# Optimization experiments

Hardware: AMD Instinct MI355X
Metric: run time of the kernel (lower is better)

The kernel has to match this reference:

```python
import jax, jax.numpy as jnp
import numpy as np

EPS = 1e-7  # K.epsilon()
ROUTINGS = 3


def squash(v, axis=-1):
    s2 = jnp.sum(jnp.square(v), axis=axis, keepdims=True)
    scale = s2 / (1.0 + s2) / jnp.sqrt(s2 + EPS)
    return scale * v


def setup_inputs() -> dict:
    key = jax.random.key(0)
    k1, k2 = jax.random.split(key)
    B, I, D, O, K = 64, 2048, 8, 32, 16
    x = jax.random.normal(k1, (B, I, D), dtype=jnp.float32)
    W = jax.random.normal(k2, (I, O, D, K), dtype=jnp.float32) * 0.05
    return {"x": x, "W": W}


def reference(x, W):
    # u_hat[b,o,i,k] = sum_d x[b,i,d] * W[i,o,d,k]
    u_hat = jnp.einsum('bid,iodk->boik', x, W)  # [B, O, I, K]
    B, O, I, _ = u_hat.shape
    b = jnp.zeros((B, O, I), dtype=u_hat.dtype)
    v = None
    for i in range(ROUTINGS):
        c = jax.nn.softmax(b, axis=1)                      # over output capsules
        s = jnp.einsum('boi,boik->bok', c, u_hat)          # weighted sum
        v = squash(s)                                      # [B, O, K]
        if i < ROUTINGS - 1:
            agreement = jnp.einsum('boik,bok->boi', u_hat, v)
            b = b + agreement
    return v
```

## Files before the change

kernel.cpp:

```cpp
#include <hip/hip_runtime.h>
#include <hip/hip_fp16.h>


typedef _Float16 hf2 __attribute__((ext_vector_type(2)));

struct __align__(16) H8 { __half2 a, b, c, d; };
struct __align__(8)  H4 { __half2 a, b; };

__device__ __forceinline__ float dot2(hf2 a, hf2 b, float c) {
#if __has_builtin(__builtin_amdgcn_fdot2)
    return __builtin_amdgcn_fdot2(a, b, c, false);
#else
    return fmaf((float)a.x, (float)b.x, fmaf((float)a.y, (float)b.y, c));
#endif
}

template<int CTRL>
__device__ __forceinline__ float dppadd(float v) {
    return v + __int_as_float(__builtin_amdgcn_update_dpp(
        0, __float_as_int(v), CTRL, 0xF, 0xF, true));
}

__global__ __launch_bounds__(512)
void prep_kernel(const float* __restrict__ W, float* __restrict__ W16)
{
    const int ch = blockIdx.x;
    const int t  = threadIdx.x;
    const int is = t >> 6, l = t & 63, o = l & 31, kk = l >> 5;
    const int i  = ch * 8 + is;

    const float* wp = W + (size_t)(i * 32 + o) * 128 + kk * 8;
    float r[8][8];
    #pragma unroll
    for (int d = 0; d < 8; ++d) {
        float4 a = *(const float4*)(wp + d * 16);
        float4 b = *(const float4*)(wp + d * 16 + 4);
        r[d][0] = a.x; r[d][1] = a.y; r[d][2] = a.z; r[d][3] = a.w;
        r[d][4] = b.x; r[d][5] = b.y; r[d][6] = b.z; r[d][7] = b.w;
    }
    float4* dst = (float4*)W16 + (size_t)i * 512 + l;
    #pragma unroll
    for (int j = 0; j < 8; ++j) {
        float o4[4];
        #pragma unroll
        for (int d2 = 0; d2 < 4; ++d2) {
            hf2 p; p.x = (_Float16)r[2 * d2][j]; p.y = (_Float16)r[2 * d2 + 1][j];
            o4[d2] = __builtin_bit_cast(float, p);
        }
        dst[(size_t)j * 64] = make_float4(o4[0], o4[1], o4[2], o4[3]);
    }
}

template<int PASS0>
__global__ __launch_bounds__(512, 6)
void pass_kernel(const float* __restrict__ x,
                 const float* __restrict__ W16,
                 const __half* __restrict__ vin,
                 __half* __restrict__ part)
{
    __shared__ __align__(16) hf2    x_ldsh[16][8][4];
    __shared__ __align__(16) __half redh[2][16][512];

    const int t  = threadIdx.x;
    const int w  = t >> 6;
    const int l  = t & 63;
    const int o  = l & 31;
    const int kk = l >> 5;
    const int bx = blockIdx.x;
    const int ch = bx & 255;
    const int qh = bx >> 8;

    float Whf[4][8];
    {
        const float4* wp = (const float4*)W16 + (size_t)(ch * 8 + w) * 512 + l;
        #pragma unroll
        for (int j = 0; j < 8; ++j) {
            float4 ld = wp[(size_t)j * 64];
            Whf[0][j] = ld.x; Whf[1][j] = ld.y; Whf[2][j] = ld.z; Whf[3][j] = ld.w;
        }
        #pragma unroll
        for (int d2 = 0; d2 < 4; ++d2)
            #pragma unroll
            for (int j = 0; j < 8; ++j)
                asm volatile("" : "+v"(Whf[d2][j]));
    }
    {
        const int bl = t >> 5, wv = (t >> 2) & 7, d2 = t & 3;
        const float2 xx = *(const float2*)(
            x + (size_t)(qh * 16 + bl) * 16384 + (size_t)(ch * 8 + wv) * 8 + 2 * d2);
        hf2 p; p.x = (_Float16)xx.x; p.y = (_Float16)xx.y;
        x_ldsh[bl][wv][d2] = p;
    }

    #pragma unroll 2
    for (int g = 0; g < 8; ++g) {
        __syncthreads();

        if (g && t < 256) {
            const int bqf = t >> 7;
            const int hx  = (t & 127) * 4;
            const __half* rp = &redh[(g - 1) & 1][0][0];
            float a0 = 0.f, a1 = 0.f, a2 = 0.f, a3 = 0.f;
            #pragma unroll
            for (int s = 0; s < 8; ++s) {
                H4 v = *(const H4*)(rp + (s * 2 + bqf) * 512 + hx);
                float2 f0 = __half22float2(v.a), f1 = __half22float2(v.b);
                a0 += f0.x; a1 += f0.y; a2 += f1.x; a3 += f1.y;
            }
            const int b = qh * 16 + (g - 1) * 2 + bqf;
            const int qq = hx >> 6, rr = hx & 63;
            H4 o4;
            o4.a = __floats2half2_rn(a0, a1);
            o4.b = __floats2half2_rn(a2, a3);
            *(H4*)(part + (((size_t)b * 8 + qq) * 256 + ch) * 64 + rr) = o4;
        }

        #pragma unroll
        for (int bq = 0; bq < 2; ++bq) {
            const int bl = g * 2 + bq;
            H8 vv;
            if (!PASS0) {
                vv = *(const H8*)(vin + (size_t)(qh * 16 + bl) * 512 + o * 16 + kk * 8);
            }
            const hf2* xp = &x_ldsh[bl][w][0];
            hf2 xa0 = xp[0], xa1 = xp[1], xa2 = xp[2], xa3 = xp[3];
            float uh[8];
            #pragma unroll
            for (int j = 0; j < 8; ++j) uh[j] = 0.f;
            #pragma unroll
            for (int j = 0; j < 8; ++j) {
                uh[j] = dot2(xa0, __builtin_bit_cast(hf2, Whf[0][j]), uh[j]);
                uh[j] = dot2(xa1, __builtin_bit_cast(hf2, Whf[1][j]), uh[j]);
                uh[j] = dot2(xa2, __builtin_bit_cast(hf2, Whf[2][j]), uh[j]);
                uh[j] = dot2(xa3, __builtin_bit_cast(hf2, Whf[3][j]), uh[j]);
            }
            float c;
            if (PASS0) {
                c = 0.03125f;
            } else {
                float2 v0 = __half22float2(vv.a), v1 = __half22float2(vv.b);
                float2 v2 = __half22float2(vv.c), v3 = __half22float2(vv.d);
                float logit = uh[0] * v0.x;
                logit = fmaf(uh[1], v0.y, logit);
                logit = fmaf(uh[2], v1.x, logit);
                logit = fmaf(uh[3], v1.y, logit);
                logit = fmaf(uh[4], v2.x, logit);
                logit = fmaf(uh[5], v2.y, logit);
                logit = fmaf(uh[6], v3.x, logit);
                logit = fmaf(uh[7], v3.y, logit);
                logit += __shfl_xor(logit, 32, 64);
                float ex = __expf(logit);
                float sm = ex;
                sm = dppadd<0xB1>(sm);
                sm = dppadd<0x4E>(sm);
                sm = dppadd<0x124>(sm);
                sm = dppadd<0x128>(sm);
                sm += __int_as_float(__builtin_amdgcn_ds_swizzle(
                          __float_as_int(sm), 0x401F));
                c = __fdividef(ex, sm);
            }
            H8 pk;
            pk.a = __floats2half2_rn(c * uh[0], c * uh[1]);
            pk.b = __floats2half2_rn(c * uh[2], c * uh[3]);
            pk.c = __floats2half2_rn(c * uh[4], c * uh[5]);
            pk.d = __floats2half2_rn(c * uh[6], c * uh[7]);
            *(H8*)&redh[g & 1][w * 2 + bq][o * 16 + kk * 8] = pk;
        }
    }
    __syncthreads();
    if (t < 256) {
        const int bqf = t >> 7;
        const int hx  = (t & 127) * 4;
        const __half* rp = &redh[1][0][0];
        float a0 = 0.f, a1 = 0.f, a2 = 0.f, a3 = 0.f;
        #pragma unroll
        for (int s = 0; s < 8; ++s) {
            H4 v = *(const H4*)(rp + (s * 2 + bqf) * 512 + hx);
            float2 f0 = __half22float2(v.a), f1 = __half22float2(v.b);
            a0 += f0.x; a1 += f0.y; a2 += f1.x; a3 += f1.y;
        }
        const int b = qh * 16 + 14 + bqf;
        const int qq = hx >> 6, rr = hx & 63;
        H4 o4;
        o4.a = __floats2half2_rn(a0, a1);
        o4.b = __floats2half2_rn(a2, a3);
        *(H4*)(part + (((size_t)b * 8 + qq) * 256 + ch) * 64 + rr) = o4;
    }
}

template<int PHASE>
__global__ __launch_bounds__(1024)
void reduce_kernel(const __half* __restrict__ part,
                   __half* __restrict__ vsum,
                   float* __restrict__ out)
{
    __shared__ float sAf[256][68];
    __shared__ float sB[16][64];
    const int bx = blockIdx.x;
    const int b  = bx >> 3;
    const int q  = bx & 7;
    const int t  = threadIdx.x;

    const __half* base = part + (((size_t)b * 8 + q) * 256) * 64;
    H8 v0 = *(const H8*)(base + t * 16);
    H8 v1 = *(const H8*)(base + t * 16 + 8);
    const int ch = t >> 2, rq = t & 3;
    float* dst = &sAf[ch][rq * 16];
    {
        float2 f;
        f = __half22float2(v0.a); dst[0]  = f.x; dst[1]  = f.y;
        f = __half22float2(v0.b); dst[2]  = f.x; dst[3]  = f.y;
        f = __half22float2(v0.c); dst[4]  = f.x; dst[5]  = f.y;
        f = __half22float2(v0.d); dst[6]  = f.x; dst[7]  = f.y;
        f = __half22float2(v1.a); dst[8]  = f.x; dst[9]  = f.y;
        f = __half22float2(v1.b); dst[10] = f.x; dst[11] = f.y;
        f = __half22float2(v1.c); dst[12] = f.x; dst[13] = f.y;
        f = __half22float2(v1.d); dst[14] = f.x; dst[15] = f.y;
    }
    __syncthreads();

    {
        const int grp = t >> 6, r = t & 63;
        float sb = 0.f;
        #pragma unroll
        for (int cc = 0; cc < 16; ++cc)
            sb += sAf[grp * 16 + cc][r];
        sB[grp][r] = sb;
    }
    __syncthreads();

    if (t < 64) {
        float s1 = 0.f;
        #pragma unroll
        for (int grp = 0; grp < 16; ++grp) s1 += sB[grp][t];
        float sq = s1 * s1;
        #pragma unroll
        for (int off = 8; off >= 1; off >>= 1)
            sq += __shfl_xor(sq, off, 16);
        float v = (sq / (1.f + sq) * rsqrtf(sq + 1e-7f)) * s1;
        const size_t idx = (size_t)b * 512 + q * 64 + t;
        if (PHASE == 2)      out[idx] = v;
        else if (PHASE == 1) vsum[idx] = __float2half((float)vsum[idx] + v);
        else                 vsum[idx] = __float2half(v);
    }
}

extern "C" void kernel_launch(void* const* d_in, const int* in_sizes, int n_in,
                              void* d_out, int out_size, void* d_ws, size_t ws_size,
                              hipStream_t stream)
{
    const float* x = (const float*)d_in[0];
    const float* W = (const float*)d_in[1];
    float* out = (float*)d_out;
    char* ws = (char*)d_ws;

    const size_t partB = (size_t)64 * 8 * 256 * 64 * 2;
    const size_t vsumB = (size_t)64 * 512 * 2;
    const size_t w16B  = (size_t)2048 * 32 * 8 * 16 * 2;
    if (ws_size < partB + vsumB + w16B) return;

    __half* part = (__half*)ws;
    __half* vsum = (__half*)(ws + partB);
    float*  W16  = (float*)(ws + partB + vsumB);

    prep_kernel<<<256, 512, 0, stream>>>(W, W16);

    pass_kernel<1><<<1024, 512, 0, stream>>>(x, W16, vsum, part);
    reduce_kernel<0><<<512, 1024, 0, stream>>>(part, vsum, out);
    pass_kernel<0><<<1024, 512, 0, stream>>>(x, W16, vsum, part);
    reduce_kernel<1><<<512, 1024, 0, stream>>>(part, vsum, out);
    pass_kernel<0><<<1024, 512, 0, stream>>>(x, W16, vsum, part);
    reduce_kernel<2><<<512, 1024, 0, stream>>>(part, vsum, out);
}
```

Measured before the change: 174.7 us.

## Restructure pass kernel: warps own batches and accumulate over input capsules in registers

Changes the work split so each wavefront handles two batch rows and loops over the block's eight input capsules, streaming W from global memory each iteration instead of keeping one capsule's weights in registers. Accumulation over capsules now happens in fp32 registers, which removes the shared-memory reduction buffer, the per-step barriers and the separate LDS reduction phase. It also lowers the occupancy hint in launch bounds. The trade-off is eight times more W global/L2 reads per block and more live registers, in exchange for fewer syncs and less LDS traffic.

Result: slower. 243.3 us (+39.3%).

```diff
diff --git a/kernel.cpp b/kernel.cpp
--- a/kernel.cpp
+++ b/kernel.cpp
@@ -14,11 +14,35 @@
     return fmaf((float)a.x, (float)b.x, fmaf((float)a.y, (float)b.y, c));
 #endif
 }
+__device__ __forceinline__ hf2 bch(float f) { return __builtin_bit_cast(hf2, f); }
 
 template<int CTRL>
 __device__ __forceinline__ float dppadd(float v) {
     return v + __int_as_float(__builtin_amdgcn_update_dpp(
         0, __float_as_int(v), CTRL, 0xF, 0xF, true));
+}
+
+__device__ __forceinline__ float softmax_c(const float uh[8], const H8& vv) {
+    float2 v0 = __half22float2(vv.a), v1 = __half22float2(vv.b);
+    float2 v2 = __half22float2(vv.c), v3 = __half22float2(vv.d);
+    float logit = uh[0] * v0.x;
+    logit = fmaf(uh[1], v0.y, logit);
+    logit = fmaf(uh[2], v1.x, logit);
+    logit = fmaf(uh[3], v1.y, logit);
+    logit = fmaf(uh[4], v2.x, logit);
+    logit = fmaf(uh[5], v2.y, logit);
+    logit = fmaf(uh[6], v3.x, logit);
+    logit = fmaf(uh[7], v3.y, logit);
+    logit += __shfl_xor(logit, 32, 64);
+    float ex = __expf(logit);
+    float sm = ex;
+    sm = dppadd<0xB1>(sm);
+    sm = dppadd<0x4E>(sm);
+    sm = dppadd<0x124>(sm);
+    sm = dppadd<0x128>(sm);
+    sm += __int_as_float(__builtin_amdgcn_ds_swizzle(
+              __float_as_int(sm), 0x401F));
+    return __fdividef(ex, sm);
 }
 
 __global__ __launch_bounds__(512)
@@ -52,14 +76,13 @@
 }
 
 template<int PASS0>
-__global__ __launch_bounds__(512, 6)
+__global__ __launch_bounds__(512, 4)
 void pass_kernel(const float* __restrict__ x,
                  const float* __restrict__ W16,
                  const __half* __restrict__ vin,
                  __half* __restrict__ part)
 {
-    __shared__ __align__(16) hf2    x_ldsh[16][8][4];
-    __shared__ __align__(16) __half redh[2][16][512];
+    __shared__ __align__(16) hf2 x_ldsh[16][8][4];
 
     const int t  = threadIdx.x;
     const int w  = t >> 6;
@@ -70,20 +93,6 @@
     const int ch = bx & 255;
     const int qh = bx >> 8;
 
-    float Whf[4][8];
-    {
-        const float4* wp = (const float4*)W16 + (size_t)(ch * 8 + w) * 512 + l;
-        #pragma unroll
-        for (int j = 0; j < 8; ++j) {
-            float4 ld = wp[(size_t)j * 64];
-            Whf[0][j] = ld.x; Whf[1][j] = ld.y; Whf[2][j] = ld.z; Whf[3][j] = ld.w;
-        }
-        #pragma unroll
-        for (int d2 = 0; d2 < 4; ++d2)
-            #pragma unroll
-            for (int j = 0; j < 8; ++j)
-                asm volatile("" : "+v"(Whf[d2][j]));
-    }
     {
         const int bl = t >> 5, wv = (t >> 2) & 7, d2 = t & 3;
         const float2 xx = *(const float2*)(
@@ -92,100 +101,70 @@
         x_ldsh[bl][wv][d2] = p;
     }
 
-    #pragma unroll 2
-    for (int g = 0; g < 8; ++g) {
-        __syncthreads();
-
-        if (g && t < 256) {
-            const int bqf = t >> 7;
-            const int hx  = (t & 127) * 4;
-            const __half* rp = &redh[(g - 1) & 1][0][0];
-            float a0 = 0.f, a1 = 0.f, a2 = 0.f, a3 = 0.f;
+    const int b0 = qh * 16 + w * 2;
+    H8 vv0, vv1;
+    if (!PASS0) {
+        vv0 = *(const H8*)(vin + (size_t)b0 * 512 + o * 16 + kk * 8);
+        vv1 = *(const H8*)(vin + (size_t)(b0 + 1) * 512 + o * 16 + kk * 8);
+    }
+    __syncthreads();
+
+    float acc0[8], acc1[8];
+    #pragma unroll
+    for (int j = 0; j < 8; ++j) { acc0[j] = 0.f; acc1[j] = 0.f; }
+
+    const float4* wbase = (const float4*)W16 + (size_t)(ch * 8) * 512 + l;
+
+    for (int i = 0; i < 8; ++i) {
+        float4 wf[8];
+        #pragma unroll
+        for (int j = 0; j < 8; ++j)
+            wf[j] = wbase[(size_t)i * 512 + (size_t)j * 64];
+
+        const hf2* xp0 = &x_ldsh[w * 2][i][0];
+        const hf2* xp1 = &x_ldsh[w * 2 + 1][i][0];
+        hf2 x00 = xp0[0], x01 = xp0[1], x02 = xp0[2], x03 = xp0[3];
+        hf2 x10 = xp1[0], x11 = xp1[1], x12 = xp1[2], x13 = xp1[3];
+
+        float uh0[8], uh1[8];
+        #pragma unroll
+        for (int j = 0; j < 8; ++j) {
+            uh0[j] = dot2(x03, bch(wf[j].w), dot2(x02, bch(wf[j].z),
+                     dot2(x01, bch(wf[j].y), dot2(x00, bch(wf[j].x), 0.f))));
+            uh1[j] = dot2(x13, bch(wf[j].w), dot2(x12, bch(wf[j].z),
+                     dot2(x11, bch(wf[j].y), dot2(x10, bch(wf[j].x), 0.f))));
+        }
+        if (PASS0) {
             #pragma unroll
-            for (int s = 0; s < 8; ++s) {
-                H4 v = *(const H4*)(rp + (s * 2 + bqf) * 512 + hx);
-                float2 f0 = __half22float2(v.a), f1 = __half22float2(v.b);
-                a0 += f0.x; a1 += f0.y; a2 += f1.x; a3 += f1.y;
-            }
-            const int b = qh * 16 + (g - 1) * 2 + bqf;
-            const int qq = hx >> 6, rr = hx & 63;
-            H4 o4;
-            o4.a = __floats2half2_rn(a0, a1);
-            o4.b = __floats2half2_rn(a2, a3);
-            *(H4*)(part + (((size_t)b * 8 + qq) * 256 + ch) * 64 + rr) = o4;
-        }
-
-        #pragma unroll
-        for (int bq = 0; bq < 2; ++bq) {
-            const int bl = g * 2 + bq;
-            H8 vv;
-            if (!PASS0) {
-                vv = *(const H8*)(vin + (size_t)(qh * 16 + bl) * 512 + o * 16 + kk * 8);
-            }
-            const hf2* xp = &x_ldsh[bl][w][0];
-            hf2 xa0 = xp[0], xa1 = xp[1], xa2 = xp[2], xa3 = xp[3];
-            float uh[8];
-            #pragma unroll
-            for (int j = 0; j < 8; ++j) uh[j] = 0.f;
+            for (int j = 0; j < 8; ++j) { acc0[j] += uh0[j]; acc1[j] += uh1[j]; }
+        } else {
+            const float c0 = softmax_c(uh0, vv0);
+            const float c1 = softmax_c(uh1, vv1);
             #pragma unroll
             for (int j = 0; j < 8; ++j) {
-                uh[j] = dot2(xa0, __builtin_bit_cast(hf2, Whf[0][j]), uh[j]);
-                uh[j] = dot2(xa1, __builtin_bit_cast(hf2, Whf[1][j]), uh[j]);
-                uh[j] = dot2(xa2, __builtin_bit_cast(hf2, Whf[2][j]), uh[j]);
-                uh[j] = dot2(xa3, __builtin_bit_cast(hf2, Whf[3][j]), uh[j]);
+                acc0[j] = fmaf(c0, uh0[j], acc0[j]);
+                acc1[j] = fmaf(c1, uh1[j], acc1[j]);
             }
-            float c;
-            if (PASS0) {
-                c = 0.03125f;
-            } else {
-                float2 v0 = __half22float2(vv.a), v1 = __half22float2(vv.b);
-                float2 v2 = __half22float2(vv.c), v3 = __half22float2(vv.d);
-                float logit = uh[0] * v0.x;
-                logit = fmaf(uh[1], v0.y, logit);
-                logit = fmaf(uh[2], v1.x, logit);
-                logit = fmaf(uh[3], v1.y, logit);
-                logit = fmaf(uh[4], v2.x, logit);
-                logit = fmaf(uh[5], v2.y, logit);
-                logit = fmaf(uh[6], v3.x, logit);
-                logit = fmaf(uh[7], v3.y, logit);
-                logit += __shfl_xor(logit, 32, 64);
-                float ex = __expf(logit);
-                float sm = ex;
-                sm = dppadd<0xB1>(sm);
-                sm = dppadd<0x4E>(sm);
-                sm = dppadd<0x124>(sm);
-                sm = dppadd<0x128>(sm);
-                sm += __int_as_float(__builtin_amdgcn_ds_swizzle(
-                          __float_as_int(sm), 0x401F));
-                c = __fdividef(ex, sm);
-            }
-            H8 pk;
-            pk.a = __floats2half2_rn(c * uh[0], c * uh[1]);
-            pk.b = __floats2half2_rn(c * uh[2], c * uh[3]);
-            pk.c = __floats2half2_rn(c * uh[4], c * uh[5]);
-            pk.d = __floats2half2_rn(c * uh[6], c * uh[7]);
-            *(H8*)&redh[g & 1][w * 2 + bq][o * 16 + kk * 8] = pk;
         }
     }
-    __syncthreads();
-    if (t < 256) {
-        const int bqf = t >> 7;
-        const int hx  = (t & 127) * 4;
-        const __half* rp = &redh[1][0][0];
-        float a0 = 0.f, a1 = 0.f, a2 = 0.f, a3 = 0.f;
-        #pragma unroll
-        for (int s = 0; s < 8; ++s) {
-            H4 v = *(const H4*)(rp + (s * 2 + bqf) * 512 + hx);
-            float2 f0 = __half22float2(v.a), f1 = __half22float2(v.b);
-            a0 += f0.x; a1 += f0.y; a2 += f1.x; a3 += f1.y;
-        }
-        const int b = qh * 16 + 14 + bqf;
-        const int qq = hx >> 6, rr = hx & 63;
-        H4 o4;
-        o4.a = __floats2half2_rn(a0, a1);
-        o4.b = __floats2half2_rn(a2, a3);
-        *(H4*)(part + (((size_t)b * 8 + qq) * 256 + ch) * 64 + rr) = o4;
-    }
+
+    if (PASS0) {
+        #pragma unroll
+        for (int j = 0; j < 8; ++j) { acc0[j] *= 0.03125f; acc1[j] *= 0.03125f; }
+    }
+    const size_t roff = (size_t)(o >> 2) * 256 * 64 + (size_t)ch * 64
+                      + (o & 3) * 16 + kk * 8;
+    H8 pk;
+    pk.a = __floats2half2_rn(acc0[0], acc0[1]);
+    pk.b = __floats2half2_rn(acc0[2], acc0[3]);
+    pk.c = __floats2half2_rn(acc0[4], acc0[5]);
+    pk.d = __floats2half2_rn(acc0[6], acc0[7]);
+    *(H8*)(part + (size_t)b0 * 8 * 256 * 64 + roff) = pk;
+    pk.a = __floats2half2_rn(acc1[0], acc1[1]);
+    pk.b = __floats2half2_rn(acc1[2], acc1[3]);
+    pk.c = __floats2half2_rn(acc1[4], acc1[5]);
+    pk.d = __floats2half2_rn(acc1[6], acc1[7]);
+    *(H8*)(part + (size_t)(b0 + 1) * 8 * 256 * 64 + roff) = pk;
 }
 
 template<int PHASE>
```
